# Kernel optimization log

Measured on AMD Instinct MI355X. Metric: run time of the kernel, lower is better.

The kernel has to match this reference:

```python
import jax, jax.numpy as jnp
import numpy as np

DIM = 768
HEADS = 12
HEAD_DIM = DIM // HEADS


def setup_inputs() -> dict:
    key = jax.random.key(0)
    ks = jax.random.split(key, 5)
    B, S = 4, 2048
    init = 0.02
    x = jax.random.normal(ks[0], (B, S, DIM), dtype=jnp.float32)
    w_qkv = jax.random.normal(ks[1], (DIM, 3 * DIM), dtype=jnp.float32) * init
    b_qkv = jnp.zeros((3 * DIM,), dtype=jnp.float32)
    w_out = jax.random.normal(ks[2], (DIM, DIM), dtype=jnp.float32) * init
    b_out = jnp.zeros((DIM,), dtype=jnp.float32)
    return {"x": x, "w_qkv": w_qkv, "b_qkv": b_qkv, "w_out": w_out, "b_out": b_out}


def reference(x, w_qkv, b_qkv, w_out, b_out):
    B, S, D = x.shape
    # QKV projection: [B,S,3D] -> [3,B,H,S,hd]
    qkv = x @ w_qkv + b_qkv
    qkv = qkv.reshape(B, S, 3, HEADS, HEAD_DIM).transpose(2, 0, 3, 1, 4)
    q, k, v = qkv[0], qkv[1], qkv[2]
    # NOTE: original scales by 1/sqrt(head_num), not 1/sqrt(head_dim)
    scale = 1.0 / jnp.sqrt(jnp.float32(HEADS))
    scores = jnp.einsum("bhqd,bhkd->bhqk", q, k) * scale
    attn = jax.nn.softmax(scores, axis=-1)
    out = jnp.einsum("bhqk,bhkd->bhqd", attn, v)
    out = out.transpose(0, 2, 1, 3).reshape(B, S, D)
    return out @ w_out + b_out
```

## Files before the change

### kernel.cpp

```cpp
#include <hip/hip_runtime.h>
#include <hip/hip_bf16.h>
#include <cstdint>
#include <cstddef>

#define HEADS 12
#define HD    64
#define NB    4
#define SEQ   2048
#define DIM   768
#define NQKV  2304

static constexpr float QSCALE = 0.2886751345948129f * 1.4426950408889634f;

typedef __attribute__((ext_vector_type(8))) short short8;
typedef __attribute__((ext_vector_type(4))) short short4v;
typedef __attribute__((ext_vector_type(4))) float f32x4;

__device__ inline unsigned short f2bf(float x) {
    union { float f; uint32_t u; } v; v.f = x;
    return (unsigned short)((v.u + 0x7fffu + ((v.u >> 16) & 1u)) >> 16);
}

__device__ inline unsigned short f2bf_fast(float x) {
    __hip_bfloat16 h = __float2bfloat16(x);
    unsigned short u;
    __builtin_memcpy(&u, &h, 2);
    return u;
}

__device__ inline void gld16(const void* g, void* l) {
    __builtin_amdgcn_global_load_lds(
        (const __attribute__((address_space(1))) unsigned int*)g,
        (__attribute__((address_space(3))) unsigned int*)l, 16, 0, 0);
}

__global__ __launch_bounds__(256) void convert_x_kernel(
    const float* __restrict__ x, unsigned short* __restrict__ xb)
{
    const size_t i = ((size_t)blockIdx.x * 256 + threadIdx.x) * 8;
    const float4 a = *reinterpret_cast<const float4*>(x + i);
    const float4 b = *reinterpret_cast<const float4*>(x + i + 4);
    short8 o;
    o[0] = (short)f2bf(a.x); o[1] = (short)f2bf(a.y);
    o[2] = (short)f2bf(a.z); o[3] = (short)f2bf(a.w);
    o[4] = (short)f2bf(b.x); o[5] = (short)f2bf(b.y);
    o[6] = (short)f2bf(b.z); o[7] = (short)f2bf(b.w);
    *reinterpret_cast<short8*>(xb + i) = o;
}

__global__ __launch_bounds__(256) void transpose_w_kernel(
    const float* __restrict__ w, unsigned short* __restrict__ wT,
    int ncols , int nrows )
{
    __shared__ float tile[64][65];
    const int k0 = blockIdx.y * 64;
    const int n0 = blockIdx.x * 64;
    const int tr = threadIdx.x >> 4;
    const int tc4 = (threadIdx.x & 15) * 4;
    #pragma unroll
    for (int it = 0; it < 4; ++it) {
        const int kk = tr + it * 16;
        *reinterpret_cast<float4*>(&tile[kk][tc4]) =
            *reinterpret_cast<const float4*>(w + (size_t)(k0 + kk) * ncols + n0 + tc4);
    }
    __syncthreads();
    #pragma unroll
    for (int it = 0; it < 4; ++it) {
        const int nn = tr + it * 16;
        short4v o;
        #pragma unroll
        for (int r = 0; r < 4; ++r) o[r] = (short)f2bf(tile[tc4 + r][nn]);
        *reinterpret_cast<short4v*>(wT + (size_t)(n0 + nn) * nrows + k0 + tc4) = o;
    }
}

__global__ __launch_bounds__(256) void qkv_gemm_bf16(
    const unsigned short* __restrict__ A,
    const unsigned short* __restrict__ BT,
    const float* __restrict__ bias,
    unsigned short* __restrict__ qb, unsigned short* __restrict__ kb,
    unsigned short* __restrict__ vt)
{
    __shared__ __align__(16) unsigned short As[128][64];
    __shared__ __align__(16) unsigned short Bs[128][64];

    const int tid = threadIdx.x;
    const int wave = tid >> 6;
    const int lane = tid & 63;
    const int col = lane & 15;
    const int g = lane >> 4;
    const int m0 = blockIdx.y * 128;
    const int n0 = blockIdx.x * 128;
    const int wr = wave >> 1, wc = wave & 1;

    const int srow = tid >> 3;
    const int scl  = tid & 7;

    f32x4 acc[4][4] = {};

    for (int kt = 0; kt < DIM; kt += 64) {
        __syncthreads();
        #pragma unroll
        for (int it = 0; it < 4; ++it) {
            const int row = srow + it * 32;
            const int cg = scl ^ (row & 7);
            gld16(A + (size_t)(m0 + row) * DIM + kt + cg * 8,
                  &As[0][0] + (size_t)(it * 256 + wave * 64) * 8);
            gld16(BT + (size_t)(n0 + row) * DIM + kt + cg * 8,
                  &Bs[0][0] + (size_t)(it * 256 + wave * 64) * 8);
        }
        __syncthreads();

        #pragma unroll
        for (int ks = 0; ks < 2; ++ks) {
            short8 af[4], bf[4];
            #pragma unroll
            for (int i = 0; i < 4; ++i) {
                const int ra = wr * 64 + i * 16 + col;
                af[i] = *reinterpret_cast<const short8*>(
                    &As[ra][(((ks * 4 + g) ^ (ra & 7)) << 3)]);
                const int rb = wc * 64 + i * 16 + col;
                bf[i] = *reinterpret_cast<const short8*>(
                    &Bs[rb][(((ks * 4 + g) ^ (rb & 7)) << 3)]);
            }
            #pragma unroll
            for (int i = 0; i < 4; ++i)
                #pragma unroll
                for (int j = 0; j < 4; ++j)
                    acc[i][j] = __builtin_amdgcn_mfma_f32_16x16x32_bf16(
                        af[i], bf[j], acc[i][j], 0, 0, 0);
        }
    }

    const int which = n0 / DIM;
    #pragma unroll
    for (int j = 0; j < 4; ++j) {
        const int n = n0 + wc * 64 + j * 16 + col;
        const int rem = n - which * DIM;
        const int h = rem >> 6, dh = rem & 63;
        const float bj = bias[n];
        #pragma unroll
        for (int i = 0; i < 4; ++i) {
            const int mbase = m0 + wr * 64 + i * 16 + g * 4;
            const int b_ = mbase >> 11;
            const int s_ = mbase & 2047;
            const size_t bh = (size_t)(b_ * HEADS + h);
            if (which == 2) {
                short4v pk;
                #pragma unroll
                for (int r = 0; r < 4; ++r)
                    pk[r] = (short)f2bf(acc[i][j][r] + bj);
                *reinterpret_cast<short4v*>(vt + (bh * HD + dh) * SEQ + s_) = pk;
            } else {
                unsigned short* dst = (which == 0) ? qb : kb;
                const float sc = (which == 0) ? QSCALE : 1.0f;
                #pragma unroll
                for (int r = 0; r < 4; ++r)
                    dst[(bh * SEQ + s_ + r) * HD + dh] =
                        f2bf((acc[i][j][r] + bj) * sc);
            }
        }
    }
}

__global__ __launch_bounds__(256) void attn_kernel(
    const unsigned short* __restrict__ qb, const unsigned short* __restrict__ kbuf,
    const unsigned short* __restrict__ vt, unsigned short* __restrict__ ctxb)
{
    __shared__ __align__(16) unsigned short Ks[2][64][64];
    __shared__ __align__(16) unsigned short Vs[2][64][64];
    __shared__ __align__(16) unsigned short Ps[4][16][64];

    const int tid = threadIdx.x;
    const int wave = tid >> 6;
    const int lane = tid & 63;
    const int col = lane & 15;
    const int g   = lane >> 4;
    const int bh = blockIdx.y;
    const int q0 = blockIdx.x * 64;
    const int wq = q0 + wave * 16 + col;

    const size_t hb = (size_t)bh * SEQ * HD;

    short8 qf[2];
    {
        const unsigned short* src = qb + hb + (size_t)wq * HD + g * 8;
        qf[0] = *reinterpret_cast<const short8*>(src);
        qf[1] = *reinterpret_cast<const short8*>(src + 32);
    }

    f32x4 acc4[4] = {};
    float l_part = 0.0f;

    const unsigned short* Kg = kbuf + hb;
    const unsigned short* Vg = vt + hb;

    const int srow = tid >> 3;
    const int sc_  = tid & 7;

    auto STAGE = [&](int jt, int bsel) {
        const int kb0 = jt * 64;
        #pragma unroll
        for (int it = 0; it < 2; ++it) {
            const int row = srow + it * 32;
            const int cg = sc_ ^ (row & 7);
            gld16(Kg + (size_t)(kb0 + row) * HD + cg * 8,
                  &Ks[bsel][0][0] + (size_t)(it * 256 + wave * 64) * 8);
            gld16(Vg + (size_t)row * SEQ + kb0 + cg * 8,
                  &Vs[bsel][0][0] + (size_t)(it * 256 + wave * 64) * 8);
        }
    };

    const int NT = SEQ / 64;
    STAGE(0, 0);

    for (int jt = 0; jt < NT; ++jt) {
        const int cur = jt & 1;
        if (jt + 1 < NT) {
            STAGE(jt + 1, cur ^ 1);
            asm volatile("s_waitcnt vmcnt(4)" ::: "memory");
        } else {
            asm volatile("s_waitcnt vmcnt(0)" ::: "memory");
        }
        __builtin_amdgcn_s_barrier();

        f32x4 st[4] = {};
        __builtin_amdgcn_s_setprio(1);
        #pragma unroll
        for (int m = 0; m < 4; ++m) {
            const int row = m * 16 + col;
            const short8 kf0 = *reinterpret_cast<const short8*>(
                &Ks[cur][row][((g ^ (row & 7)) << 3)]);
            const short8 kf1 = *reinterpret_cast<const short8*>(
                &Ks[cur][row][(((g + 4) ^ (row & 7)) << 3)]);
            st[m] = __builtin_amdgcn_mfma_f32_16x16x32_bf16(kf0, qf[0], st[m], 0, 0, 0);
            st[m] = __builtin_amdgcn_mfma_f32_16x16x32_bf16(kf1, qf[1], st[m], 0, 0, 0);
        }
        __builtin_amdgcn_s_setprio(0);

        float s0 = 0.0f, s1 = 0.0f, s2 = 0.0f, s3 = 0.0f;
        #pragma unroll
        for (int m = 0; m < 4; ++m) {
            float p[4];
            p[0] = __builtin_amdgcn_exp2f(st[m][0]);
            p[1] = __builtin_amdgcn_exp2f(st[m][1]);
            p[2] = __builtin_amdgcn_exp2f(st[m][2]);
            p[3] = __builtin_amdgcn_exp2f(st[m][3]);
            s0 += p[0]; s1 += p[1]; s2 += p[2]; s3 += p[3];
            short4v pk;
            #pragma unroll
            for (int r = 0; r < 4; ++r) pk[r] = (short)f2bf_fast(p[r]);
            const int scw = (2 * m + (g >> 1)) ^ (col & 7);
            *reinterpret_cast<short4v*>(
                &Ps[wave][col][(scw << 3) + ((g & 1) << 2)]) = pk;
        }
        l_part += (s0 + s1) + (s2 + s3);

        const short8 pf0 = *reinterpret_cast<const short8*>(
            &Ps[wave][col][((g ^ (col & 7)) << 3)]);
        const short8 pf1 = *reinterpret_cast<const short8*>(
            &Ps[wave][col][(((g + 4) ^ (col & 7)) << 3)]);

        __builtin_amdgcn_s_setprio(1);
        #pragma unroll
        for (int nb = 0; nb < 4; ++nb) {
            const int row = nb * 16 + col;
            const short8 vf0 = *reinterpret_cast<const short8*>(
                &Vs[cur][row][((g ^ (row & 7)) << 3)]);
            const short8 vf1 = *reinterpret_cast<const short8*>(
                &Vs[cur][row][(((g + 4) ^ (row & 7)) << 3)]);
            acc4[nb] = __builtin_amdgcn_mfma_f32_16x16x32_bf16(pf0, vf0, acc4[nb], 0, 0, 0);
            acc4[nb] = __builtin_amdgcn_mfma_f32_16x16x32_bf16(pf1, vf1, acc4[nb], 0, 0, 0);
        }
        __builtin_amdgcn_s_setprio(0);

        __builtin_amdgcn_s_barrier();
    }

    float lt = l_part + __shfl_xor(l_part, 16);
    lt += __shfl_xor(lt, 32);
    float lr[4];
    #pragma unroll
    for (int r = 0; r < 4; ++r) lr[r] = 1.0f / __shfl(lt, g * 4 + r);
    const int b_ = bh / HEADS;
    const int h = bh - b_ * HEADS;
    #pragma unroll
    for (int nb = 0; nb < 4; ++nb)
        #pragma unroll
        for (int r = 0; r < 4; ++r) {
            const int s_ = q0 + wave * 16 + g * 4 + r;
            ctxb[((size_t)b_ * SEQ + s_) * DIM + h * HD + nb * 16 + col] =
                f2bf_fast(acc4[nb][r] * lr[r]);
        }
}

__global__ __launch_bounds__(256) void out_gemm_bf16(
    const unsigned short* __restrict__ A,
    const unsigned short* __restrict__ BT,
    const float* __restrict__ bias, float* __restrict__ out)
{
    __shared__ __align__(16) unsigned short As[128][64];
    __shared__ __align__(16) unsigned short Bs[128][64];

    const int tid = threadIdx.x;
    const int wave = tid >> 6;
    const int lane = tid & 63;
    const int col = lane & 15;
    const int g = lane >> 4;
    const int m0 = blockIdx.y * 128;
    const int n0 = blockIdx.x * 128;
    const int wr = wave >> 1, wc = wave & 1;

    const int srow = tid >> 3;
    const int scl  = tid & 7;

    f32x4 acc[4][4] = {};

    for (int kt = 0; kt < DIM; kt += 64) {
        __syncthreads();
        #pragma unroll
        for (int it = 0; it < 4; ++it) {
            const int row = srow + it * 32;
            const int cg = scl ^ (row & 7);
            gld16(A + (size_t)(m0 + row) * DIM + kt + cg * 8,
                  &As[0][0] + (size_t)(it * 256 + wave * 64) * 8);
            gld16(BT + (size_t)(n0 + row) * DIM + kt + cg * 8,
                  &Bs[0][0] + (size_t)(it * 256 + wave * 64) * 8);
        }
        __syncthreads();

        #pragma unroll
        for (int ks = 0; ks < 2; ++ks) {
            short8 af[4], bf[4];
            #pragma unroll
            for (int i = 0; i < 4; ++i) {
                const int ra = wr * 64 + i * 16 + col;
                af[i] = *reinterpret_cast<const short8*>(
                    &As[ra][(((ks * 4 + g) ^ (ra & 7)) << 3)]);
                const int rb = wc * 64 + i * 16 + col;
                bf[i] = *reinterpret_cast<const short8*>(
                    &Bs[rb][(((ks * 4 + g) ^ (rb & 7)) << 3)]);
            }
            #pragma unroll
            for (int i = 0; i < 4; ++i)
                #pragma unroll
                for (int j = 0; j < 4; ++j)
                    acc[i][j] = __builtin_amdgcn_mfma_f32_16x16x32_bf16(
                        af[i], bf[j], acc[i][j], 0, 0, 0);
        }
    }

    #pragma unroll
    for (int j = 0; j < 4; ++j) {
        const int n = n0 + wc * 64 + j * 16 + col;
        const float bj = bias[n];
        #pragma unroll
        for (int i = 0; i < 4; ++i) {
            const int m = m0 + wr * 64 + i * 16 + g * 4;
            #pragma unroll
            for (int r = 0; r < 4; ++r)
                out[(size_t)(m + r) * DIM + n] = acc[i][j][r] + bj;
        }
    }
}

extern "C" void kernel_launch(void* const* d_in, const int* in_sizes, int n_in,
                              void* d_out, int out_size, void* d_ws, size_t ws_size,
                              hipStream_t stream)
{
    const float* x     = (const float*)d_in[0];
    const float* w_qkv = (const float*)d_in[1];
    const float* b_qkv = (const float*)d_in[2];
    const float* w_out = (const float*)d_in[3];
    const float* b_out = (const float*)d_in[4];
    float* out = (float*)d_out;

    const size_t QSZ = (size_t)NB * HEADS * SEQ * HD;
    unsigned short* qb   = (unsigned short*)d_ws;
    unsigned short* kb   = qb + QSZ;
    unsigned short* vt   = kb + QSZ;
    unsigned short* xb   = vt + QSZ;
    unsigned short* ctxb = xb + QSZ;
    unsigned short* wqT  = ctxb + QSZ;
    unsigned short* woT  = wqT + (size_t)NQKV * DIM;

    convert_x_kernel<<<3072, 256, 0, stream>>>(x, xb);
    transpose_w_kernel<<<dim3(NQKV / 64, DIM / 64), 256, 0, stream>>>(
        w_qkv, wqT, NQKV, DIM);
    transpose_w_kernel<<<dim3(DIM / 64, DIM / 64), 256, 0, stream>>>(
        w_out, woT, DIM, DIM);

    qkv_gemm_bf16<<<dim3(NQKV / 128, (NB * SEQ) / 128), 256, 0, stream>>>(
        xb, wqT, b_qkv, qb, kb, vt);
    attn_kernel<<<dim3(SEQ / 64, NB * HEADS), 256, 0, stream>>>(qb, kb, vt, ctxb);
    out_gemm_bf16<<<dim3(DIM / 128, (NB * SEQ) / 128), 256, 0, stream>>>(
        ctxb, woT, b_out, out);
}
```

Before: 173.8 us.

## Use 32x32 MFMA with register-resident P in attention kernel

```diff
diff --git a/kernel.cpp b/kernel.cpp
--- a/kernel.cpp
+++ b/kernel.cpp
@@ -15,6 +15,8 @@
 typedef __attribute__((ext_vector_type(8))) short short8;
 typedef __attribute__((ext_vector_type(4))) short short4v;
 typedef __attribute__((ext_vector_type(4))) float f32x4;
+typedef __attribute__((ext_vector_type(16))) float f32x16;
+typedef __attribute__((ext_vector_type(4))) unsigned int u32x4;
 
 __device__ inline unsigned short f2bf(float x) {
     union { float f; uint32_t u; } v; v.f = x;
@@ -169,45 +171,44 @@
 {
     __shared__ __align__(16) unsigned short Ks[2][64][64];
     __shared__ __align__(16) unsigned short Vs[2][64][64];
-    __shared__ __align__(16) unsigned short Ps[4][16][64];
 
     const int tid = threadIdx.x;
-    const int wave = tid >> 6;
+    const int wv   = tid >> 6;
     const int lane = tid & 63;
-    const int col = lane & 15;
-    const int g   = lane >> 4;
-    const int bh = blockIdx.y;
-    const int q0 = blockIdx.x * 64;
-    const int wq = q0 + wave * 16 + col;
+    const int col  = lane & 31;
+    const int half = lane >> 5;
+
+    const int bid = blockIdx.x;
+    const int vbid = (bid & 7) * 96 + (bid >> 3);
+    const int bh = vbid >> 4;
+    const int q0 = (vbid & 15) * 128;
+    const int wq = q0 + wv * 32 + col;
 
     const size_t hb = (size_t)bh * SEQ * HD;
 
-    short8 qf[2];
-    {
-        const unsigned short* src = qb + hb + (size_t)wq * HD + g * 8;
-        qf[0] = *reinterpret_cast<const short8*>(src);
-        qf[1] = *reinterpret_cast<const short8*>(src + 32);
-    }
-
-    f32x4 acc4[4] = {};
+    short8 qf[4];
+    #pragma unroll
+    for (int stp = 0; stp < 4; ++stp)
+        qf[stp] = *reinterpret_cast<const short8*>(
+            qb + hb + (size_t)wq * HD + stp * 16 + half * 8);
+
+    f32x16 acc0 = {}, acc1 = {};
     float l_part = 0.0f;
 
     const unsigned short* Kg = kbuf + hb;
     const unsigned short* Vg = vt + hb;
 
-    const int srow = tid >> 3;
-    const int sc_  = tid & 7;
-
     auto STAGE = [&](int jt, int bsel) {
         const int kb0 = jt * 64;
         #pragma unroll
         for (int it = 0; it < 2; ++it) {
-            const int row = srow + it * 32;
-            const int cg = sc_ ^ (row & 7);
+            const int slot = tid + it * 256;
+            const int row = slot >> 3;
+            const int cg = (slot & 7) ^ (row & 7);
             gld16(Kg + (size_t)(kb0 + row) * HD + cg * 8,
-                  &Ks[bsel][0][0] + (size_t)(it * 256 + wave * 64) * 8);
+                  &Ks[bsel][0][0] + (size_t)slot * 8);
             gld16(Vg + (size_t)row * SEQ + kb0 + cg * 8,
-                  &Vs[bsel][0][0] + (size_t)(it * 256 + wave * 64) * 8);
+                  &Vs[bsel][0][0] + (size_t)slot * 8);
         }
     };
 
@@ -224,74 +225,91 @@
         }
         __builtin_amdgcn_s_barrier();
 
-        f32x4 st[4] = {};
+        f32x16 st0 = {}, st1 = {};
         __builtin_amdgcn_s_setprio(1);
         #pragma unroll
-        for (int m = 0; m < 4; ++m) {
-            const int row = m * 16 + col;
+        for (int stp = 0; stp < 4; ++stp) {
+            const int r0 = col;
             const short8 kf0 = *reinterpret_cast<const short8*>(
-                &Ks[cur][row][((g ^ (row & 7)) << 3)]);
+                &Ks[cur][r0][(((2 * stp + half) ^ (r0 & 7)) << 3)]);
+            st0 = __builtin_amdgcn_mfma_f32_32x32x16_bf16(kf0, qf[stp], st0, 0, 0, 0);
+            const int r1 = 32 + col;
             const short8 kf1 = *reinterpret_cast<const short8*>(
-                &Ks[cur][row][(((g + 4) ^ (row & 7)) << 3)]);
-            st[m] = __builtin_amdgcn_mfma_f32_16x16x32_bf16(kf0, qf[0], st[m], 0, 0, 0);
-            st[m] = __builtin_amdgcn_mfma_f32_16x16x32_bf16(kf1, qf[1], st[m], 0, 0, 0);
+                &Ks[cur][r1][(((2 * stp + half) ^ (r1 & 7)) << 3)]);
+            st1 = __builtin_amdgcn_mfma_f32_32x32x16_bf16(kf1, qf[stp], st1, 0, 0, 0);
         }
         __builtin_amdgcn_s_setprio(0);
 
-        float s0 = 0.0f, s1 = 0.0f, s2 = 0.0f, s3 = 0.0f;
-        #pragma unroll
-        for (int m = 0; m < 4; ++m) {
-            float p[4];
-            p[0] = __builtin_amdgcn_exp2f(st[m][0]);
-            p[1] = __builtin_amdgcn_exp2f(st[m][1]);
-            p[2] = __builtin_amdgcn_exp2f(st[m][2]);
-            p[3] = __builtin_amdgcn_exp2f(st[m][3]);
-            s0 += p[0]; s1 += p[1]; s2 += p[2]; s3 += p[3];
-            short4v pk;
-            #pragma unroll
-            for (int r = 0; r < 4; ++r) pk[r] = (short)f2bf_fast(p[r]);
-            const int scw = (2 * m + (g >> 1)) ^ (col & 7);
-            *reinterpret_cast<short4v*>(
-                &Ps[wave][col][(scw << 3) + ((g & 1) << 2)]) = pk;
-        }
-        l_part += (s0 + s1) + (s2 + s3);
-
-        const short8 pf0 = *reinterpret_cast<const short8*>(
-            &Ps[wave][col][((g ^ (col & 7)) << 3)]);
-        const short8 pf1 = *reinterpret_cast<const short8*>(
-            &Ps[wave][col][(((g + 4) ^ (col & 7)) << 3)]);
+        unsigned int u0[8], u1[8];
+        {
+            float p[16];
+            #pragma unroll
+            for (int r = 0; r < 16; ++r) p[r] = __builtin_amdgcn_exp2f(st0[r]);
+            #pragma unroll
+            for (int r = 0; r < 16; ++r) l_part += p[r];
+            #pragma unroll
+            for (int j = 0; j < 8; ++j)
+                asm("v_cvt_pk_bf16_f32 %0, %1, %2"
+                    : "=v"(u0[j]) : "v"(p[2 * j]), "v"(p[2 * j + 1]));
+            #pragma unroll
+            for (int r = 0; r < 16; ++r) p[r] = __builtin_amdgcn_exp2f(st1[r]);
+            #pragma unroll
+            for (int r = 0; r < 16; ++r) l_part += p[r];
+            #pragma unroll
+            for (int j = 0; j < 8; ++j)
+                asm("v_cvt_pk_bf16_f32 %0, %1, %2"
+                    : "=v"(u1[j]) : "v"(p[2 * j]), "v"(p[2 * j + 1]));
+        }
+        #pragma unroll
+        for (int t = 0; t < 2; ++t) {
+            asm volatile("v_permlane32_swap_b32 %0, %1" : "+v"(u0[t]), "+v"(u0[t + 2]));
+            asm volatile("v_permlane32_swap_b32 %0, %1" : "+v"(u0[t + 4]), "+v"(u0[t + 6]));
+            asm volatile("v_permlane32_swap_b32 %0, %1" : "+v"(u1[t]), "+v"(u1[t + 2]));
+            asm volatile("v_permlane32_swap_b32 %0, %1" : "+v"(u1[t + 4]), "+v"(u1[t + 6]));
+        }
+        short8 pw[4];
+        {
+            u32x4 w;
+            w = (u32x4){u0[0], u0[1], u0[2], u0[3]}; __builtin_memcpy(&pw[0], &w, 16);
+            w = (u32x4){u0[4], u0[5], u0[6], u0[7]}; __builtin_memcpy(&pw[1], &w, 16);
+            w = (u32x4){u1[0], u1[1], u1[2], u1[3]}; __builtin_memcpy(&pw[2], &w, 16);
+            w = (u32x4){u1[4], u1[5], u1[6], u1[7]}; __builtin_memcpy(&pw[3], &w, 16);
+        }
 
         __builtin_amdgcn_s_setprio(1);
         #pragma unroll
-        for (int nb = 0; nb < 4; ++nb) {
-            const int row = nb * 16 + col;
+        for (int ks = 0; ks < 4; ++ks) {
+            const int r0 = col;
             const short8 vf0 = *reinterpret_cast<const short8*>(
-                &Vs[cur][row][((g ^ (row & 7)) << 3)]);
+                &Vs[cur][r0][(((2 * ks + half) ^ (r0 & 7)) << 3)]);
+            acc0 = __builtin_amdgcn_mfma_f32_32x32x16_bf16(vf0, pw[ks], acc0, 0, 0, 0);
+            const int r1 = 32 + col;
             const short8 vf1 = *reinterpret_cast<const short8*>(
-                &Vs[cur][row][(((g + 4) ^ (row & 7)) << 3)]);
-            acc4[nb] = __builtin_amdgcn_mfma_f32_16x16x32_bf16(pf0, vf0, acc4[nb], 0, 0, 0);
-            acc4[nb] = __builtin_amdgcn_mfma_f32_16x16x32_bf16(pf1, vf1, acc4[nb], 0, 0, 0);
+                &Vs[cur][r1][(((2 * ks + half) ^ (r1 & 7)) << 3)]);
+            acc1 = __builtin_amdgcn_mfma_f32_32x32x16_bf16(vf1, pw[ks], acc1, 0, 0, 0);
         }
         __builtin_amdgcn_s_setprio(0);
 
         __builtin_amdgcn_s_barrier();
     }
 
-    float lt = l_part + __shfl_xor(l_part, 16);
-    lt += __shfl_xor(lt, 32);
-    float lr[4];
-    #pragma unroll
-    for (int r = 0; r < 4; ++r) lr[r] = 1.0f / __shfl(lt, g * 4 + r);
+    const float lt = l_part + __shfl_xor(l_part, 32);
+    const float inv = 1.0f / lt;
     const int b_ = bh / HEADS;
     const int h = bh - b_ * HEADS;
-    #pragma unroll
-    for (int nb = 0; nb < 4; ++nb)
-        #pragma unroll
-        for (int r = 0; r < 4; ++r) {
-            const int s_ = q0 + wave * 16 + g * 4 + r;
-            ctxb[((size_t)b_ * SEQ + s_) * DIM + h * HD + nb * 16 + col] =
-                f2bf_fast(acc4[nb][r] * lr[r]);
-        }
+    const int s_ = q0 + wv * 32 + col;
+    unsigned short* dst = ctxb + ((size_t)b_ * SEQ + s_) * DIM + h * HD;
+    #pragma unroll
+    for (int a = 0; a < 4; ++a) {
+        short4v o0, o1;
+        #pragma unroll
+        for (int e = 0; e < 4; ++e) {
+            o0[e] = (short)f2bf_fast(acc0[4 * a + e] * inv);
+            o1[e] = (short)f2bf_fast(acc1[4 * a + e] * inv);
+        }
+        *reinterpret_cast<short4v*>(dst + a * 8 + half * 4) = o0;
+        *reinterpret_cast<short4v*>(dst + 32 + a * 8 + half * 4) = o1;
+    }
 }
 
 __global__ __launch_bounds__(256) void out_gemm_bf16(
@@ -392,7 +410,7 @@
 
     qkv_gemm_bf16<<<dim3(NQKV / 128, (NB * SEQ) / 128), 256, 0, stream>>>(
         xb, wqT, b_qkv, qb, kb, vt);
-    attn_kernel<<<dim3(SEQ / 64, NB * HEADS), 256, 0, stream>>>(qb, kb, vt, ctxb);
+    attn_kernel<<<dim3((SEQ / 128) * NB * HEADS), 256, 0, stream>>>(qb, kb, vt, ctxb);
     out_gemm_bf16<<<dim3(DIM / 128, (NB * SEQ) / 128), 256, 0, stream>>>(
         ctxb, woT, b_out, out);
 }
```

New measurement: 158.3 us. 1.1x faster.
